# Kernel tuning notes

Measured on AMD Instinct MI355X. Metric: run time of the kernel, lower is better.

The kernel has to match this reference:

```python
import jax, jax.numpy as jnp
import numpy as np

D = 128
NUM_STRUCTURES = 8
N = 1024
BERNOULLI_INIT = 0.5


def setup_inputs() -> dict:
    key = jax.random.key(0)
    k_x, k_m, k_w = jax.random.split(key, 3)
    x = jax.random.normal(k_x, (N, D), dtype=jnp.float32)
    # maskings: 0/1 DAG masks (one per structure), float for multiplication
    maskings = jax.random.randint(k_m, (NUM_STRUCTURES, D, D), 0, 2).astype(jnp.float32)
    # Bernoulli logits/probs theta, initialized at bernouilli_init
    theta = jnp.full((NUM_STRUCTURES, D, D), BERNOULLI_INIT, dtype=jnp.float32)
    # Linear structural-equation weights
    W = jax.random.normal(k_w, (NUM_STRUCTURES, D, D), dtype=jnp.float32)
    return {"x": x, "maskings": maskings, "theta": theta, "W": W}


def _bernoulli_ste(theta):
    # BernoulliSTERoot: hard Bernoulli sample with straight-through estimator.
    # Fixed noise key for deterministic reference.
    u = jax.random.uniform(jax.random.key(42), theta.shape, dtype=theta.dtype)
    hard = (u < theta).astype(theta.dtype)
    return theta + jax.lax.stop_gradient(hard - theta)


def reference(x, maskings, theta, W):
    # dags[o,p,c]: masked Bernoulli sample of edge p->c for structure o
    dags = maskings * _bernoulli_ste(theta)  # (o, d, d)
    # masked_x[o,n,c,p] = dags[o,p,c] * x[n,p]  (large 4-D intermediate, as in original)
    masked_x = jnp.einsum('opc,np->oncp', dags, x)  # (o, n, d, d)
    # x_hat[o,n,c] = sum_p masked_x[o,n,c,p] * W[o,p,c]
    x_hat = jnp.einsum('oncp,opc->onc', masked_x, W)  # (o, n, d)
    return x_hat
```

## Files before the change

kernel.cpp:

```cpp
#include <hip/hip_runtime.h>
#include <stdint.h>

#define NSTRUCT 8
#define NROWS   1024
#define DD      128


__device__ __forceinline__ uint32_t rotl32(uint32_t x, uint32_t d) {
  return (x << d) | (x >> (32u - d));
}

__global__ __launch_bounds__(256) void build_M(
    const float* __restrict__ maskings,
    const float* __restrict__ theta,
    const float* __restrict__ W,
    float* __restrict__ M) {
  uint32_t i = blockIdx.x * 256u + threadIdx.x;

  const uint32_t ks0 = 0u;
  const uint32_t ks1 = 42u;
  const uint32_t ks2 = 0x1BD11BDAu ^ ks0 ^ ks1;

  uint32_t x0 = 0u + ks0;
  uint32_t x1 = i  + ks1;

#define TF_RND(r) { x0 += x1; x1 = rotl32(x1, r); x1 ^= x0; }
  TF_RND(13) TF_RND(15) TF_RND(26) TF_RND(6)
  x0 += ks1; x1 += ks2 + 1u;
  TF_RND(17) TF_RND(29) TF_RND(16) TF_RND(24)
  x0 += ks2; x1 += ks0 + 2u;
  TF_RND(13) TF_RND(15) TF_RND(26) TF_RND(6)
  x0 += ks0; x1 += ks1 + 3u;
  TF_RND(17) TF_RND(29) TF_RND(16) TF_RND(24)
  x0 += ks1; x1 += ks2 + 4u;
  TF_RND(13) TF_RND(15) TF_RND(26) TF_RND(6)
  x0 += ks2; x1 += ks0 + 5u;
#undef TF_RND

  uint32_t bits = x0 ^ x1;
  float u = __uint_as_float((bits >> 9) | 0x3f800000u) - 1.0f;
  M[i] = (u < theta[i]) ? maskings[i] * W[i] : 0.0f;
}


__global__ __launch_bounds__(256) void sem_gemm(
    const float* __restrict__ x,
    const float* __restrict__ M,
    float* __restrict__ out) {
  __shared__ float xs[32 * DD];
  __shared__ float Ms[32 * DD];

  const int o   = blockIdx.x >> 5;
  const int n0  = (blockIdx.x & 31) << 5;
  const int tid = threadIdx.x;
  const int r0  = (tid >> 5) << 2;
  const int c0  = (tid & 31) << 2;

  {
    const float4* src = (const float4*)(x + n0 * DD);
    float4* dst = (float4*)xs;
#pragma unroll
    for (int k = 0; k < 4; ++k) dst[tid + k * 256] = src[tid + k * 256];
  }

  float acc[4][4];
#pragma unroll
  for (int a = 0; a < 4; ++a)
#pragma unroll
    for (int b = 0; b < 4; ++b) acc[a][b] = 0.0f;

  const float4* msrcBase = (const float4*)(M + o * DD * DD);

  for (int p0 = 0; p0 < DD; p0 += 32) {
    __syncthreads();
    {
      const float4* src = msrcBase + (p0 * DD) / 4;
      float4* dst = (float4*)Ms;
#pragma unroll
      for (int k = 0; k < 4; ++k) dst[tid + k * 256] = src[tid + k * 256];
    }
    __syncthreads();

#pragma unroll 8
    for (int pp = 0; pp < 32; ++pp) {
      float4 b = *(const float4*)&Ms[pp * DD + c0];
      float a0 = xs[(r0 + 0) * DD + p0 + pp];
      float a1 = xs[(r0 + 1) * DD + p0 + pp];
      float a2 = xs[(r0 + 2) * DD + p0 + pp];
      float a3 = xs[(r0 + 3) * DD + p0 + pp];
      acc[0][0] += a0 * b.x; acc[0][1] += a0 * b.y; acc[0][2] += a0 * b.z; acc[0][3] += a0 * b.w;
      acc[1][0] += a1 * b.x; acc[1][1] += a1 * b.y; acc[1][2] += a1 * b.z; acc[1][3] += a1 * b.w;
      acc[2][0] += a2 * b.x; acc[2][1] += a2 * b.y; acc[2][2] += a2 * b.z; acc[2][3] += a2 * b.w;
      acc[3][0] += a3 * b.x; acc[3][1] += a3 * b.y; acc[3][2] += a3 * b.z; acc[3][3] += a3 * b.w;
    }
  }

  float* obase = out + ((size_t)o * NROWS + n0) * DD;
#pragma unroll
  for (int a = 0; a < 4; ++a) {
    float4 v = make_float4(acc[a][0], acc[a][1], acc[a][2], acc[a][3]);
    *(float4*)&obase[(r0 + a) * DD + c0] = v;
  }
}


extern "C" void kernel_launch(void* const* d_in, const int* in_sizes, int n_in,
                              void* d_out, int out_size, void* d_ws, size_t ws_size,
                              hipStream_t stream) {
  const float* x        = (const float*)d_in[0];
  const float* maskings = (const float*)d_in[1];
  const float* theta    = (const float*)d_in[2];
  const float* W        = (const float*)d_in[3];
  float* out = (float*)d_out;
  float* M   = (float*)d_ws;

  build_M<<<(NSTRUCT * DD * DD) / 256, 256, 0, stream>>>(maskings, theta, W, M);
  sem_gemm<<<NSTRUCT * (NROWS / 32), 256, 0, stream>>>(x, M, out);
}
```

Baseline: 69.48 us.

## Fuse mask construction into the GEMM kernel with transposed swizzled x tile

Merges the two kernels into one. Each block regenerates its 128x32 slice of the masked weight matrix (Threefry RNG, theta compare, mask times W) straight into shared memory, so the intermediate M no longer goes through global memory and one launch is dropped. The tiling changes to 128 rows by 32 columns per block, with x stored transposed in shared memory using an XOR swizzle so the inner loop reads float4 vectors. In exchange, each M slice is recomputed by the 8 row-tile blocks, only 256 blocks are launched, and each uses about 80KB of LDS with launch bounds of 1, so occupancy is low.

```diff
diff --git a/kernel.cpp b/kernel.cpp
--- a/kernel.cpp
+++ b/kernel.cpp
@@ -10,20 +10,12 @@
   return (x << d) | (x >> (32u - d));
 }
 
-__global__ __launch_bounds__(256) void build_M(
-    const float* __restrict__ maskings,
-    const float* __restrict__ theta,
-    const float* __restrict__ W,
-    float* __restrict__ M) {
-  uint32_t i = blockIdx.x * 256u + threadIdx.x;
-
+__device__ __forceinline__ uint32_t threefry_bits(uint32_t i) {
   const uint32_t ks0 = 0u;
   const uint32_t ks1 = 42u;
   const uint32_t ks2 = 0x1BD11BDAu ^ ks0 ^ ks1;
-
   uint32_t x0 = 0u + ks0;
   uint32_t x1 = i  + ks1;
-
 #define TF_RND(r) { x0 += x1; x1 = rotl32(x1, r); x1 ^= x0; }
   TF_RND(13) TF_RND(15) TF_RND(26) TF_RND(6)
   x0 += ks1; x1 += ks2 + 1u;
@@ -36,73 +28,82 @@
   TF_RND(13) TF_RND(15) TF_RND(26) TF_RND(6)
   x0 += ks2; x1 += ks0 + 5u;
 #undef TF_RND
-
-  uint32_t bits = x0 ^ x1;
-  float u = __uint_as_float((bits >> 9) | 0x3f800000u) - 1.0f;
-  M[i] = (u < theta[i]) ? maskings[i] * W[i] : 0.0f;
+  return x0 ^ x1;
 }
 
+__global__ __launch_bounds__(256, 1) void nnl0_fused(
+    const float* __restrict__ x,
+    const float* __restrict__ maskings,
+    const float* __restrict__ theta,
+    const float* __restrict__ W,
+    float* __restrict__ out) {
+  __shared__ float Ms[DD * 32];
+  __shared__ float xs[DD * DD];
 
-__global__ __launch_bounds__(256) void sem_gemm(
-    const float* __restrict__ x,
-    const float* __restrict__ M,
-    float* __restrict__ out) {
-  __shared__ float xs[32 * DD];
-  __shared__ float Ms[32 * DD];
-
-  const int o   = blockIdx.x >> 5;
-  const int n0  = (blockIdx.x & 31) << 5;
+  const int b   = blockIdx.x;
+  const int o   = b >> 5;
+  const int cq  = (b >> 3) & 3;
+  const int rt  = b & 7;
+  const int n0  = rt << 7;
+  const int cb  = cq << 5;
   const int tid = threadIdx.x;
-  const int r0  = (tid >> 5) << 2;
-  const int c0  = (tid & 31) << 2;
 
   {
-    const float4* src = (const float4*)(x + n0 * DD);
-    float4* dst = (float4*)xs;
-#pragma unroll
-    for (int k = 0; k < 4; ++k) dst[tid + k * 256] = src[tid + k * 256];
+    const int mbase = o * DD * DD;
+#pragma unroll 2
+    for (int k = 0; k < 16; ++k) {
+      int idx = k * 256 + tid;
+      int p = idx >> 5;
+      int c = idx & 31;
+      int gi = mbase + p * DD + cb + c;
+      uint32_t bits = threefry_bits((uint32_t)gi);
+      float u = __uint_as_float((bits >> 9) | 0x3f800000u) - 1.0f;
+      float v = (u < theta[gi]) ? maskings[gi] * W[gi] : 0.0f;
+      Ms[p * 32 + c] = v;
+    }
   }
+
+#pragma unroll 2
+  for (int k = 0; k < 16; ++k) {
+    int q = k * 256 + tid;
+    int n = q >> 5;
+    int pc = (q & 31) << 2;
+    float4 v = *(const float4*)&x[(size_t)(n0 + n) * DD + pc];
+    int g = n >> 2, nj = n & 3;
+    xs[(pc + 0) * DD + ((g ^ ((pc + 0) & 31)) << 2) + nj] = v.x;
+    xs[(pc + 1) * DD + ((g ^ ((pc + 1) & 31)) << 2) + nj] = v.y;
+    xs[(pc + 2) * DD + ((g ^ ((pc + 2) & 31)) << 2) + nj] = v.z;
+    xs[(pc + 3) * DD + ((g ^ ((pc + 3) & 31)) << 2) + nj] = v.w;
+  }
+
+  __syncthreads();
+
+  const int c0 = (tid & 7) << 2;
+  const int g  = tid >> 3;
 
   float acc[4][4];
 #pragma unroll
   for (int a = 0; a < 4; ++a)
 #pragma unroll
-    for (int b = 0; b < 4; ++b) acc[a][b] = 0.0f;
+    for (int bb = 0; bb < 4; ++bb) acc[a][bb] = 0.0f;
 
-  const float4* msrcBase = (const float4*)(M + o * DD * DD);
-
-  for (int p0 = 0; p0 < DD; p0 += 32) {
-    __syncthreads();
-    {
-      const float4* src = msrcBase + (p0 * DD) / 4;
-      float4* dst = (float4*)Ms;
-#pragma unroll
-      for (int k = 0; k < 4; ++k) dst[tid + k * 256] = src[tid + k * 256];
-    }
-    __syncthreads();
-
-#pragma unroll 8
-    for (int pp = 0; pp < 32; ++pp) {
-      float4 b = *(const float4*)&Ms[pp * DD + c0];
-      float a0 = xs[(r0 + 0) * DD + p0 + pp];
-      float a1 = xs[(r0 + 1) * DD + p0 + pp];
-      float a2 = xs[(r0 + 2) * DD + p0 + pp];
-      float a3 = xs[(r0 + 3) * DD + p0 + pp];
-      acc[0][0] += a0 * b.x; acc[0][1] += a0 * b.y; acc[0][2] += a0 * b.z; acc[0][3] += a0 * b.w;
-      acc[1][0] += a1 * b.x; acc[1][1] += a1 * b.y; acc[1][2] += a1 * b.z; acc[1][3] += a1 * b.w;
-      acc[2][0] += a2 * b.x; acc[2][1] += a2 * b.y; acc[2][2] += a2 * b.z; acc[2][3] += a2 * b.w;
-      acc[3][0] += a3 * b.x; acc[3][1] += a3 * b.y; acc[3][2] += a3 * b.z; acc[3][3] += a3 * b.w;
-    }
+#pragma unroll 4
+  for (int p = 0; p < DD; ++p) {
+    float4 bv = *(const float4*)&Ms[p * 32 + c0];
+    float4 av = *(const float4*)&xs[p * DD + ((g ^ (p & 31)) << 2)];
+    acc[0][0] += av.x * bv.x; acc[0][1] += av.x * bv.y; acc[0][2] += av.x * bv.z; acc[0][3] += av.x * bv.w;
+    acc[1][0] += av.y * bv.x; acc[1][1] += av.y * bv.y; acc[1][2] += av.y * bv.z; acc[1][3] += av.y * bv.w;
+    acc[2][0] += av.z * bv.x; acc[2][1] += av.z * bv.y; acc[2][2] += av.z * bv.z; acc[2][3] += av.z * bv.w;
+    acc[3][0] += av.w * bv.x; acc[3][1] += av.w * bv.y; acc[3][2] += av.w * bv.z; acc[3][3] += av.w * bv.w;
   }
 
-  float* obase = out + ((size_t)o * NROWS + n0) * DD;
+  float* obase = out + ((size_t)o * NROWS + n0 + g * 4) * DD + cb + c0;
 #pragma unroll
-  for (int a = 0; a < 4; ++a) {
-    float4 v = make_float4(acc[a][0], acc[a][1], acc[a][2], acc[a][3]);
-    *(float4*)&obase[(r0 + a) * DD + c0] = v;
+  for (int j = 0; j < 4; ++j) {
+    *(float4*)&obase[(size_t)j * DD] =
+        make_float4(acc[j][0], acc[j][1], acc[j][2], acc[j][3]);
   }
 }
-
 
 extern "C" void kernel_launch(void* const* d_in, const int* in_sizes, int n_in,
                               void* d_out, int out_size, void* d_ws, size_t ws_size,
@@ -112,8 +113,6 @@
   const float* theta    = (const float*)d_in[2];
   const float* W        = (const float*)d_in[3];
   float* out = (float*)d_out;
-  float* M   = (float*)d_ws;
 
-  build_M<<<(NSTRUCT * DD * DD) / 256, 256, 0, stream>>>(maskings, theta, W, M);
-  sem_gemm<<<NSTRUCT * (NROWS / 32), 256, 0, stream>>>(x, M, out);
+  nnl0_fused<<<NSTRUCT * 4 * 8, 256, 0, stream>>>(x, maskings, theta, W, out);
 }
```

After: 78.09 us. 12.4% more time.

## Load whole M matrix into LDS once and halve row tile per block

Applied to the files above, without the earlier changes.

The GEMM kernel now copies the full 128x128 M slice for a structure into shared memory in one pass, which removes the three extra sync/reload rounds over the K dimension. The row tile shrinks from 32 to 16, doubling the grid to 512 blocks, and each thread now computes 2x4 outputs using float4 loads along K. This raises LDS use to about 72KB per block, so occupancy is limited despite the launch-bounds hint of 2. The 2x4 tile also lowers arithmetic intensity per LDS read.

```diff
diff --git a/kernel.cpp b/kernel.cpp
--- a/kernel.cpp
+++ b/kernel.cpp
@@ -43,64 +43,60 @@
 }
 
 
-__global__ __launch_bounds__(256) void sem_gemm(
+__global__ __launch_bounds__(256, 2) void sem_gemm(
     const float* __restrict__ x,
     const float* __restrict__ M,
     float* __restrict__ out) {
-  __shared__ float xs[32 * DD];
-  __shared__ float Ms[32 * DD];
+  __shared__ float Ms[DD * DD];
+  __shared__ float xs[16 * DD];
 
-  const int o   = blockIdx.x >> 5;
-  const int n0  = (blockIdx.x & 31) << 5;
+  const int o   = blockIdx.x >> 6;
+  const int n0  = (blockIdx.x & 63) << 4;
   const int tid = threadIdx.x;
-  const int r0  = (tid >> 5) << 2;
-  const int c0  = (tid & 31) << 2;
 
   {
-    const float4* src = (const float4*)(x + n0 * DD);
+    const float4* src = (const float4*)(M + (size_t)o * DD * DD);
+    float4* dst = (float4*)Ms;
+#pragma unroll
+    for (int k = 0; k < 16; ++k) dst[tid + k * 256] = src[tid + k * 256];
+  }
+  {
+    const float4* src = (const float4*)(x + (size_t)n0 * DD);
     float4* dst = (float4*)xs;
 #pragma unroll
-    for (int k = 0; k < 4; ++k) dst[tid + k * 256] = src[tid + k * 256];
+    for (int k = 0; k < 2; ++k) dst[tid + k * 256] = src[tid + k * 256];
+  }
+  __syncthreads();
+
+  const int c0 = (tid & 31) << 2;
+  const int r0 = (tid >> 5) << 1;
+
+  float acc0[4] = {0.f, 0.f, 0.f, 0.f};
+  float acc1[4] = {0.f, 0.f, 0.f, 0.f};
+
+#pragma unroll 4
+  for (int p0 = 0; p0 < DD; p0 += 4) {
+    float4 a0 = *(const float4*)&xs[(r0 + 0) * DD + p0];
+    float4 a1 = *(const float4*)&xs[(r0 + 1) * DD + p0];
+    float4 b0 = *(const float4*)&Ms[(p0 + 0) * DD + c0];
+    float4 b1 = *(const float4*)&Ms[(p0 + 1) * DD + c0];
+    float4 b2 = *(const float4*)&Ms[(p0 + 2) * DD + c0];
+    float4 b3 = *(const float4*)&Ms[(p0 + 3) * DD + c0];
+
+    acc0[0] += a0.x * b0.x; acc0[1] += a0.x * b0.y; acc0[2] += a0.x * b0.z; acc0[3] += a0.x * b0.w;
+    acc0[0] += a0.y * b1.x; acc0[1] += a0.y * b1.y; acc0[2] += a0.y * b1.z; acc0[3] += a0.y * b1.w;
+    acc0[0] += a0.z * b2.x; acc0[1] += a0.z * b2.y; acc0[2] += a0.z * b2.z; acc0[3] += a0.z * b2.w;
+    acc0[0] += a0.w * b3.x; acc0[1] += a0.w * b3.y; acc0[2] += a0.w * b3.z; acc0[3] += a0.w * b3.w;
+
+    acc1[0] += a1.x * b0.x; acc1[1] += a1.x * b0.y; acc1[2] += a1.x * b0.z; acc1[3] += a1.x * b0.w;
+    acc1[0] += a1.y * b1.x; acc1[1] += a1.y * b1.y; acc1[2] += a1.y * b1.z; acc1[3] += a1.y * b1.w;
+    acc1[0] += a1.z * b2.x; acc1[1] += a1.z * b2.y; acc1[2] += a1.z * b2.z; acc1[3] += a1.z * b2.w;
+    acc1[0] += a1.w * b3.x; acc1[1] += a1.w * b3.y; acc1[2] += a1.w * b3.z; acc1[3] += a1.w * b3.w;
   }
 
-  float acc[4][4];
-#pragma unroll
-  for (int a = 0; a < 4; ++a)
-#pragma unroll
-    for (int b = 0; b < 4; ++b) acc[a][b] = 0.0f;
-
-  const float4* msrcBase = (const float4*)(M + o * DD * DD);
-
-  for (int p0 = 0; p0 < DD; p0 += 32) {
-    __syncthreads();
-    {
-      const float4* src = msrcBase + (p0 * DD) / 4;
-      float4* dst = (float4*)Ms;
-#pragma unroll
-      for (int k = 0; k < 4; ++k) dst[tid + k * 256] = src[tid + k * 256];
-    }
-    __syncthreads();
-
-#pragma unroll 8
-    for (int pp = 0; pp < 32; ++pp) {
-      float4 b = *(const float4*)&Ms[pp * DD + c0];
-      float a0 = xs[(r0 + 0) * DD + p0 + pp];
-      float a1 = xs[(r0 + 1) * DD + p0 + pp];
-      float a2 = xs[(r0 + 2) * DD + p0 + pp];
-      float a3 = xs[(r0 + 3) * DD + p0 + pp];
-      acc[0][0] += a0 * b.x; acc[0][1] += a0 * b.y; acc[0][2] += a0 * b.z; acc[0][3] += a0 * b.w;
-      acc[1][0] += a1 * b.x; acc[1][1] += a1 * b.y; acc[1][2] += a1 * b.z; acc[1][3] += a1 * b.w;
-      acc[2][0] += a2 * b.x; acc[2][1] += a2 * b.y; acc[2][2] += a2 * b.z; acc[2][3] += a2 * b.w;
-      acc[3][0] += a3 * b.x; acc[3][1] += a3 * b.y; acc[3][2] += a3 * b.z; acc[3][3] += a3 * b.w;
-    }
-  }
-
-  float* obase = out + ((size_t)o * NROWS + n0) * DD;
-#pragma unroll
-  for (int a = 0; a < 4; ++a) {
-    float4 v = make_float4(acc[a][0], acc[a][1], acc[a][2], acc[a][3]);
-    *(float4*)&obase[(r0 + a) * DD + c0] = v;
-  }
+  float* obase = out + ((size_t)o * NROWS + n0 + r0) * DD + c0;
+  *(float4*)&obase[0]  = make_float4(acc0[0], acc0[1], acc0[2], acc0[3]);
+  *(float4*)&obase[DD] = make_float4(acc1[0], acc1[1], acc1[2], acc1[3]);
 }
 
 
@@ -115,5 +111,5 @@
   float* M   = (float*)d_ws;
 
   build_M<<<(NSTRUCT * DD * DD) / 256, 256, 0, stream>>>(maskings, theta, W, M);
-  sem_gemm<<<NSTRUCT * (NROWS / 32), 256, 0, stream>>>(x, M, out);
+  sem_gemm<<<NSTRUCT * (NROWS / 16), 256, 0, stream>>>(x, M, out);
 }
```

Measured after the change: 68.45 us. No clear change (-1.5%).

## Switch SEM GEMM to bf16 MFMA with prepacked fragment layouts

Applied to the files above, without the earlier changes.

Replaces the fp32 LDS-tiled FMA GEMM with bf16 MFMA 16x16x32 instructions. A prep kernel builds the masked weight matrix and converts both M and x to bf16, storing them in per-lane fragment order. The GEMM kernel then loads fragments directly from global memory without shared memory or barriers. This cuts compute and load cost but reduces input precision to bf16, which may exceed tolerance for an fp32 reference.

```diff
diff --git a/kernel.cpp b/kernel.cpp
--- a/kernel.cpp
+++ b/kernel.cpp
@@ -5,25 +5,19 @@
 #define NROWS   1024
 #define DD      128
 
+typedef short bf16x8 __attribute__((ext_vector_type(8)));
+typedef float f32x4  __attribute__((ext_vector_type(4)));
 
 __device__ __forceinline__ uint32_t rotl32(uint32_t x, uint32_t d) {
   return (x << d) | (x >> (32u - d));
 }
 
-__global__ __launch_bounds__(256) void build_M(
-    const float* __restrict__ maskings,
-    const float* __restrict__ theta,
-    const float* __restrict__ W,
-    float* __restrict__ M) {
-  uint32_t i = blockIdx.x * 256u + threadIdx.x;
-
+__device__ __forceinline__ uint32_t threefry_bits(uint32_t i) {
   const uint32_t ks0 = 0u;
   const uint32_t ks1 = 42u;
   const uint32_t ks2 = 0x1BD11BDAu ^ ks0 ^ ks1;
-
   uint32_t x0 = 0u + ks0;
   uint32_t x1 = i  + ks1;
-
 #define TF_RND(r) { x0 += x1; x1 = rotl32(x1, r); x1 ^= x0; }
   TF_RND(13) TF_RND(15) TF_RND(26) TF_RND(6)
   x0 += ks1; x1 += ks2 + 1u;
@@ -36,70 +30,92 @@
   TF_RND(13) TF_RND(15) TF_RND(26) TF_RND(6)
   x0 += ks2; x1 += ks0 + 5u;
 #undef TF_RND
-
-  uint32_t bits = x0 ^ x1;
-  float u = __uint_as_float((bits >> 9) | 0x3f800000u) - 1.0f;
-  M[i] = (u < theta[i]) ? maskings[i] * W[i] : 0.0f;
+  return x0 ^ x1;
 }
 
+__device__ __forceinline__ uint16_t f32_to_bf16_rne(float v) {
+  uint32_t fb = __float_as_uint(v);
+  uint32_t lsb = (fb >> 16) & 1u;
+  return (uint16_t)((fb + 0x7fffu + lsb) >> 16);
+}
 
-__global__ __launch_bounds__(256) void sem_gemm(
+__global__ __launch_bounds__(256) void build_frags(
     const float* __restrict__ x,
-    const float* __restrict__ M,
+    const float* __restrict__ maskings,
+    const float* __restrict__ theta,
+    const float* __restrict__ W,
+    uint16_t* __restrict__ Mb,
+    uint16_t* __restrict__ xb) {
+  const int b = blockIdx.x;
+  const int tid = threadIdx.x;
+  if (b < 512) {
+    uint32_t flat = (uint32_t)b * 256u + tid;
+    uint32_t j    = flat & 7u;
+    uint32_t lane = (flat >> 3) & 63u;
+    uint32_t kk   = (flat >> 9) & 3u;
+    uint32_t ct   = (flat >> 11) & 7u;
+    uint32_t o    = flat >> 14;
+    uint32_t p = kk * 32u + (lane >> 4) * 8u + j;
+    uint32_t c = ct * 16u + (lane & 15u);
+    uint32_t gi = (o << 14) | (p << 7) | c;
+    uint32_t bits = threefry_bits(gi);
+    float u = __uint_as_float((bits >> 9) | 0x3f800000u) - 1.0f;
+    float v = (u < theta[gi]) ? maskings[gi] * W[gi] : 0.0f;
+    Mb[flat] = f32_to_bf16_rne(v);
+  } else {
+    uint32_t idx  = (uint32_t)(b - 512) * 256u + tid;
+    uint32_t j    = idx & 7u;
+    uint32_t lane = (idx >> 3) & 63u;
+    uint32_t kk   = (idx >> 9) & 3u;
+    uint32_t rt   = idx >> 11;
+    uint32_t n = rt * 16u + (lane & 15u);
+    uint32_t k = kk * 32u + (lane >> 4) * 8u + j;
+    xb[idx] = f32_to_bf16_rne(x[n * DD + k]);
+  }
+}
+
+__global__ __launch_bounds__(256) void sem_mfma(
+    const uint16_t* __restrict__ Mb,
+    const uint16_t* __restrict__ xb,
     float* __restrict__ out) {
-  __shared__ float xs[32 * DD];
-  __shared__ float Ms[32 * DD];
+  const int bidx = blockIdx.x;
+  const int o    = bidx >> 5;
+  const int rb   = bidx & 31;
+  const int tid  = threadIdx.x;
+  const int w    = tid >> 6;
+  const int lane = tid & 63;
+  const int rt_g = rb * 2 + (w & 1);
+  const int ctb  = (w >> 1) * 4;
 
-  const int o   = blockIdx.x >> 5;
-  const int n0  = (blockIdx.x & 31) << 5;
-  const int tid = threadIdx.x;
-  const int r0  = (tid >> 5) << 2;
-  const int c0  = (tid & 31) << 2;
+  const bf16x8* xbv = (const bf16x8*)xb;
+  const bf16x8* mbv = (const bf16x8*)Mb;
 
-  {
-    const float4* src = (const float4*)(x + n0 * DD);
-    float4* dst = (float4*)xs;
+  bf16x8 a[4];
 #pragma unroll
-    for (int k = 0; k < 4; ++k) dst[tid + k * 256] = src[tid + k * 256];
-  }
+  for (int kk = 0; kk < 4; ++kk) a[kk] = xbv[(rt_g * 4 + kk) * 64 + lane];
 
-  float acc[4][4];
+  f32x4 acc[4] = {{0.f, 0.f, 0.f, 0.f}, {0.f, 0.f, 0.f, 0.f},
+                  {0.f, 0.f, 0.f, 0.f}, {0.f, 0.f, 0.f, 0.f}};
+
 #pragma unroll
-  for (int a = 0; a < 4; ++a)
+  for (int t = 0; t < 4; ++t) {
+    const int ct = ctb + t;
 #pragma unroll
-    for (int b = 0; b < 4; ++b) acc[a][b] = 0.0f;
-
-  const float4* msrcBase = (const float4*)(M + o * DD * DD);
-
-  for (int p0 = 0; p0 < DD; p0 += 32) {
-    __syncthreads();
-    {
-      const float4* src = msrcBase + (p0 * DD) / 4;
-      float4* dst = (float4*)Ms;
-#pragma unroll
-      for (int k = 0; k < 4; ++k) dst[tid + k * 256] = src[tid + k * 256];
-    }
-    __syncthreads();
-
-#pragma unroll 8
-    for (int pp = 0; pp < 32; ++pp) {
-      float4 b = *(const float4*)&Ms[pp * DD + c0];
-      float a0 = xs[(r0 + 0) * DD + p0 + pp];
-      float a1 = xs[(r0 + 1) * DD + p0 + pp];
-      float a2 = xs[(r0 + 2) * DD + p0 + pp];
-      float a3 = xs[(r0 + 3) * DD + p0 + pp];
-      acc[0][0] += a0 * b.x; acc[0][1] += a0 * b.y; acc[0][2] += a0 * b.z; acc[0][3] += a0 * b.w;
-      acc[1][0] += a1 * b.x; acc[1][1] += a1 * b.y; acc[1][2] += a1 * b.z; acc[1][3] += a1 * b.w;
-      acc[2][0] += a2 * b.x; acc[2][1] += a2 * b.y; acc[2][2] += a2 * b.z; acc[2][3] += a2 * b.w;
-      acc[3][0] += a3 * b.x; acc[3][1] += a3 * b.y; acc[3][2] += a3 * b.z; acc[3][3] += a3 * b.w;
+    for (int kk = 0; kk < 4; ++kk) {
+      bf16x8 bfrag = mbv[((o * 8 + ct) * 4 + kk) * 64 + lane];
+      acc[t] = __builtin_amdgcn_mfma_f32_16x16x32_bf16(a[kk], bfrag, acc[t], 0, 0, 0);
     }
   }
 
-  float* obase = out + ((size_t)o * NROWS + n0) * DD;
+  const int col0     = lane & 15;
+  const int row_base = rb * 32 + (w & 1) * 16 + (lane >> 4) * 4;
 #pragma unroll
-  for (int a = 0; a < 4; ++a) {
-    float4 v = make_float4(acc[a][0], acc[a][1], acc[a][2], acc[a][3]);
-    *(float4*)&obase[(r0 + a) * DD + c0] = v;
+  for (int t = 0; t < 4; ++t) {
+    const int col = (ctb + t) * 16 + col0;
+#pragma unroll
+    for (int r = 0; r < 4; ++r) {
+      out[((size_t)o * NROWS + row_base + r) * DD + col] = acc[t][r];
+    }
   }
 }
 
@@ -112,8 +128,10 @@
   const float* theta    = (const float*)d_in[2];
   const float* W        = (const float*)d_in[3];
   float* out = (float*)d_out;
-  float* M   = (float*)d_ws;
 
-  build_M<<<(NSTRUCT * DD * DD) / 256, 256, 0, stream>>>(maskings, theta, W, M);
-  sem_gemm<<<NSTRUCT * (NROWS / 32), 256, 0, stream>>>(x, M, out);
+  uint16_t* Mb = (uint16_t*)d_ws;
+  uint16_t* xb = Mb + NSTRUCT * DD * DD;
+
+  build_frags<<<1024, 256, 0, stream>>>(x, maskings, theta, W, Mb, xb);
+  sem_mfma<<<NSTRUCT * 32, 256, 0, stream>>>(Mb, xb, out);
 }
```

Result: faster. 62.58 us (-9.9%).
